# Performance work log

Hardware: AMD Instinct MI355X
Metric: run time of the kernel (lower is better)

The kernel has to match this reference:

```python
import jax, jax.numpy as jnp
import numpy as np

SLOPE = 25.0  # snntorch fast_sigmoid default surrogate slope

@jax.custom_vjp
def spike(u):
    return (u > 0).astype(u.dtype)

def _spike_fwd(u):
    return spike(u), u

def _spike_bwd(u, g):
    return (g / (1.0 + SLOPE * jnp.abs(u)) ** 2,)

spike.defvjp(_spike_fwd, _spike_bwd)

def fake_quant(W):
    # brevitas-style int8 per-tensor symmetric fake-quant with STE
    s = jnp.max(jnp.abs(W)) / 127.0
    q = jnp.clip(jnp.round(W / s), -127.0, 127.0) * s
    return W + jax.lax.stop_gradient(q - W)

def setup_inputs() -> dict:
    key = jax.random.key(0)
    ks = jax.random.split(key, 8)
    B, NIN, T = 256, 512, 256
    H1, H2, OUT = 512, 512, 128
    data = jax.random.normal(ks[0], (B, NIN, T), dtype=jnp.float32)
    W1 = jax.random.normal(ks[1], (H1, NIN), dtype=jnp.float32) / np.sqrt(NIN)
    W2 = jax.random.normal(ks[2], (H2, H1), dtype=jnp.float32) / np.sqrt(H1)
    Wrec = jax.random.normal(ks[3], (H2, H2), dtype=jnp.float32) / np.sqrt(H2)
    W3 = jax.random.normal(ks[4], (OUT, H2), dtype=jnp.float32) / np.sqrt(H2)
    beta = jnp.float32(0.9)
    th = jnp.float32(1.0)
    return {"data": data, "W1": W1, "W2": W2, "Wrec": Wrec, "W3": W3,
            "beta1": beta, "th1": th, "beta_r": beta, "th_r": th,
            "beta2": beta, "th2": th}

def reference(data, W1, W2, Wrec, W3, beta1, th1, beta_r, th_r, beta2, th2):
    B = data.shape[0]
    H1, H2, OUT = W1.shape[0], W2.shape[0], W3.shape[0]
    W1q = fake_quant(W1)
    W2q = fake_quant(W2)
    Wrq = fake_quant(Wrec)
    W3q = fake_quant(W3)
    b1 = jnp.clip(beta1, 0.0, 1.0)
    br = jnp.clip(beta_r, 0.0, 1.0)
    b2 = jnp.clip(beta2, 0.0, 1.0)
    # time-major input: [T, B, NIN]
    xs = jnp.transpose(data, (2, 0, 1))

    def step(carry, x):
        m1, mr, sr, m2 = carry
        # leaky1: reset zero, reset_delay=False
        m1 = b1 * m1 + x @ W1q.T
        s1 = spike(m1 - th1)
        m1 = m1 * (1.0 - s1)
        # recurrent LIF (RLeaky-like), reset zero, reset_delay=True:
        # previous spike resets the membrane at the start of this step
        h = s1 @ W2q.T + sr @ Wrq.T
        mr = (br * mr + h) * (1.0 - sr)
        sr = spike(mr - th_r)
        # leaky2: reset zero, reset_delay=False
        m2 = b2 * m2 + sr @ W3q.T
        s2 = spike(m2 - th2)
        m2 = m2 * (1.0 - s2)
        return (m1, mr, sr, m2), s2

    init = (jnp.zeros((B, H1), jnp.float32),
            jnp.zeros((B, H2), jnp.float32),
            jnp.zeros((B, H2), jnp.float32),
            jnp.zeros((B, OUT), jnp.float32))
    _, spk_rec = jax.lax.scan(step, init, xs)
    return spk_rec  # [T, B, OUT]
```

## Files before the change

kernel.cpp:

```cpp
#include <hip/hip_runtime.h>

#define B_   256
#define NIN_ 512
#define T_   256
#define H1_  512
#define H2_  512
#define OUT_ 128

typedef __attribute__((ext_vector_type(8))) short bf16x8;
typedef __attribute__((ext_vector_type(4))) float f32x4;
typedef __attribute__((address_space(1))) const unsigned int* gl_cu;
typedef __attribute__((address_space(3))) unsigned int* ls_u;

__global__ void absmax_k(const float* __restrict__ W1, const float* __restrict__ W2,
                         const float* __restrict__ Wr, const float* __restrict__ W3,
                         float* __restrict__ scales) {
  const float* W; int n;
  switch (blockIdx.x) {
    case 0:  W = W1; n = H1_ * NIN_; break;
    case 1:  W = W2; n = H2_ * H1_;  break;
    case 2:  W = Wr; n = H2_ * H2_;  break;
    default: W = W3; n = OUT_ * H2_; break;
  }
  int tid = threadIdx.x;
  float m = 0.f;
  const float4* W4 = (const float4*)W;
  int n4 = n >> 2;
  for (int i = tid; i < n4; i += 256) {
    float4 v = W4[i];
    m = fmaxf(m, fmaxf(fmaxf(fabsf(v.x), fabsf(v.y)), fmaxf(fabsf(v.z), fabsf(v.w))));
  }
  __shared__ float red[256];
  red[tid] = m;
  __syncthreads();
  for (int s = 128; s > 0; s >>= 1) {
    if (tid < s) red[tid] = fmaxf(red[tid], red[tid + s]);
    __syncthreads();
  }
  if (tid == 0) scales[blockIdx.x] = red[0] / 127.0f;
}

__global__ void quant_all_k(const float* __restrict__ W1, const float* __restrict__ W2,
                            const float* __restrict__ Wr, const float* __restrict__ W3,
                            const float* __restrict__ scales,
                            float* __restrict__ W1qT, ushort* __restrict__ W2bf,
                            signed char* __restrict__ WrT, ushort* __restrict__ W3bf) {
  const int blk = blockIdx.x;
  if (blk < 1024) {
    int idx = blk * 256 + threadIdx.x;
    int h = idx & (H1_ - 1), i = idx >> 9;
    float s = scales[0];
    float q = rintf(W1[h * NIN_ + i] / s);
    q = fminf(fmaxf(q, -127.f), 127.f);
    W1qT[idx] = q * s;
  } else if (blk < 2048) {
    int idx = (blk - 1024) * 256 + threadIdx.x;
    float s = scales[1];
    float q = rintf(W2[idx] / s);
    q = fminf(fmaxf(q, -127.f), 127.f);
    W2bf[idx] = (ushort)(__float_as_uint(q) >> 16);
  } else if (blk < 3072) {
    int idx = (blk - 2048) * 256 + threadIdx.x;
    int r = idx >> 9, c = idx & (H2_ - 1);
    float s = scales[2];
    float q = rintf(Wr[idx] / s);
    q = fminf(fmaxf(q, -127.f), 127.f);
    WrT[(size_t)c * H2_ + r] = (signed char)q;
  } else {
    int idx = (blk - 3072) * 256 + threadIdx.x;
    float s = scales[3];
    float q = rintf(W3[idx] / s);
    q = fminf(fmaxf(q, -127.f), 127.f);
    W3bf[idx] = (ushort)(__float_as_uint(q) >> 16);
  }
}

__global__ __launch_bounds__(512, 6) void gemm_cur1_k(const float* __restrict__ data,
                                                      const float* __restrict__ W1qT,
                                                      float* __restrict__ cur1) {
  const int b  = blockIdx.y;
  const int t0 = (blockIdx.x >> 2) << 7;
  const int h0 = (blockIdx.x & 3) << 7;
  const int tid = threadIdx.x;

  __shared__ float As[2][16][128];
  __shared__ float Bs[2][16][128];

  const int ty = tid >> 4, tx = tid & 15;
  const int wv = tid >> 6;
  const int ln = tid & 63;

  float acc[4][8];
#pragma unroll
  for (int i = 0; i < 4; i++)
#pragma unroll
    for (int j = 0; j < 8; j++) acc[i][j] = 0.f;

  const float* dbase = data + (size_t)b * NIN_ * T_;

  auto issue = [&](int kb, int buf) {
    const int kr = (wv << 1) + (ln >> 5);
    const float* ga = dbase + (size_t)(kb + kr) * T_ + t0 + ((ln & 31) << 2);
    __builtin_amdgcn_global_load_lds((gl_cu)ga, (ls_u)&As[buf][wv << 1][0], 16, 0, 0);
    const float* gb = W1qT + (size_t)(kb + kr) * H1_ + h0 + ((ln & 31) << 2);
    __builtin_amdgcn_global_load_lds((gl_cu)gb, (ls_u)&Bs[buf][wv << 1][0], 16, 0, 0);
  };

  issue(0, 0);

  for (int p = 0; p < 32; p++) {
    const int cur = p & 1;
    __syncthreads();
    if (p < 31) issue((p + 1) << 4, cur ^ 1);
#pragma unroll
    for (int k = 0; k < 16; k++) {
      float4 A0 = *(const float4*)&As[cur][k][ty * 4];
      float4 B0 = *(const float4*)&Bs[cur][k][tx * 4];
      float4 B1 = *(const float4*)&Bs[cur][k][64 + tx * 4];
      float a[4] = {A0.x, A0.y, A0.z, A0.w};
      float w[8] = {B0.x, B0.y, B0.z, B0.w, B1.x, B1.y, B1.z, B1.w};
#pragma unroll
      for (int i = 0; i < 4; i++)
#pragma unroll
        for (int j = 0; j < 8; j++)
          acc[i][j] = fmaf(a[i], w[j], acc[i][j]);
    }
  }

#pragma unroll
  for (int i = 0; i < 4; i++) {
    int row = ty * 4 + i;
    float* op = cur1 + (size_t)(t0 + row) * (B_ * H1_) + (size_t)b * H1_ + h0;
    float4 cA = {acc[i][0], acc[i][1], acc[i][2], acc[i][3]};
    float4 cB = {acc[i][4], acc[i][5], acc[i][6], acc[i][7]};
    *(float4*)(op + tx * 4)      = cA;
    *(float4*)(op + 64 + tx * 4) = cB;
  }
}

__global__ __launch_bounds__(256) void scan1_k(const float* __restrict__ cur1,
                                               unsigned char* __restrict__ s1u,
                                               const float* __restrict__ beta1p,
                                               const float* __restrict__ th1p) {
  const int n = blockIdx.x * 256 + threadIdx.x;
  const float b1 = fminf(fmaxf(beta1p[0], 0.f), 1.f);
  const float th1 = th1p[0];
  const size_t S = (size_t)B_ * H1_;
  float m1 = 0.f;
  for (int t = 0; t < T_; t += 4) {
    float c0 = cur1[(size_t)t * S + n];
    float c1 = cur1[(size_t)(t + 1) * S + n];
    float c2 = cur1[(size_t)(t + 2) * S + n];
    float c3 = cur1[(size_t)(t + 3) * S + n];
    m1 = b1 * m1 + c0; bool s0 = m1 - th1 > 0.f; if (s0) m1 = 0.f;
    s1u[(size_t)t * S + n] = s0;
    m1 = b1 * m1 + c1; bool s1 = m1 - th1 > 0.f; if (s1) m1 = 0.f;
    s1u[(size_t)(t + 1) * S + n] = s1;
    m1 = b1 * m1 + c2; bool s2 = m1 - th1 > 0.f; if (s2) m1 = 0.f;
    s1u[(size_t)(t + 2) * S + n] = s2;
    m1 = b1 * m1 + c3; bool s3 = m1 - th1 > 0.f; if (s3) m1 = 0.f;
    s1u[(size_t)(t + 3) * S + n] = s3;
  }
}

__global__ __launch_bounds__(256) void gemm_spk_k(const unsigned char* __restrict__ A8,
                                                  const ushort* __restrict__ Bw,
                                                  float* __restrict__ C, int N) {
  __shared__ short As[128 * 72];
  __shared__ short Bs[128 * 72];
  const int tid = threadIdx.x;
  const int m0 = blockIdx.y << 7;
  const int n0 = blockIdx.x << 7;
  const int lane = tid & 63, wave = tid >> 6;
  const int quad = lane >> 4, lm = lane & 15;
  const int wm = wave << 5;

  f32x4 acc[2][8];
#pragma unroll
  for (int s = 0; s < 2; s++)
#pragma unroll
    for (int n = 0; n < 8; n++) acc[s][n] = (f32x4){0.f, 0.f, 0.f, 0.f};

  for (int kb = 0; kb < 512; kb += 64) {
    uint4 av[2], bv[4];
#pragma unroll
    for (int i = 0; i < 2; i++) {
      int ch = tid + (i << 8);
      int row = ch >> 2, offB = (ch & 3) << 4;
      av[i] = *(const uint4*)(A8 + (size_t)(m0 + row) * 512 + kb + offB);
    }
#pragma unroll
    for (int i = 0; i < 4; i++) {
      int ch = tid + (i << 8);
      int row = ch >> 3, off = (ch & 7) << 3;
      bv[i] = *(const uint4*)(Bw + (size_t)(n0 + row) * 512 + kb + off);
    }
    __syncthreads();
#pragma unroll
    for (int i = 0; i < 2; i++) {
      int ch = tid + (i << 8);
      int row = ch >> 2, offB = (ch & 3) << 4;
      unsigned u[4] = {av[i].x, av[i].y, av[i].z, av[i].w};
      unsigned d[8];
#pragma unroll
      for (int w = 0; w < 4; w++) {
        unsigned uu = u[w];
        d[2 * w]     = ((uu & 1u) | ((uu & 0x100u) << 8)) * 0x3F80u;
        d[2 * w + 1] = (((uu >> 16) & 1u) | ((uu & 0x1000000u) >> 8)) * 0x3F80u;
      }
      uint4* dst = (uint4*)&As[row * 72 + offB];
      dst[0] = make_uint4(d[0], d[1], d[2], d[3]);
      dst[1] = make_uint4(d[4], d[5], d[6], d[7]);
    }
#pragma unroll
    for (int i = 0; i < 4; i++) {
      int ch = tid + (i << 8);
      int row = ch >> 3, off = (ch & 7) << 3;
      *(uint4*)&Bs[row * 72 + off] = bv[i];
    }
    __syncthreads();
#pragma unroll
    for (int kc = 0; kc < 64; kc += 32) {
      bf16x8 af0 = *(const bf16x8*)&As[(wm + lm) * 72 + kc + quad * 8];
      bf16x8 af1 = *(const bf16x8*)&As[(wm + 16 + lm) * 72 + kc + quad * 8];
      bf16x8 bfr[8];
#pragma unroll
      for (int n = 0; n < 8; n++)
        bfr[n] = *(const bf16x8*)&Bs[((n << 4) + lm) * 72 + kc + quad * 8];
#pragma unroll
      for (int n = 0; n < 8; n++) {
        acc[0][n] = __builtin_amdgcn_mfma_f32_16x16x32_bf16(af0, bfr[n], acc[0][n], 0, 0, 0);
        acc[1][n] = __builtin_amdgcn_mfma_f32_16x16x32_bf16(af1, bfr[n], acc[1][n], 0, 0, 0);
      }
    }
    __syncthreads();
  }

#pragma unroll
  for (int s = 0; s < 2; s++)
#pragma unroll
    for (int n = 0; n < 8; n++) {
      int row = m0 + wm + (s << 4) + quad * 4;
      int col = n0 + (n << 4) + lm;
#pragma unroll
      for (int r = 0; r < 4; r++)
        C[(size_t)(row + r) * N + col] = acc[s][n][r];
    }
}

__device__ __forceinline__ void unp_add(unsigned w, int* a) {
  int iw = (int)w;
  a[0] += (iw << 24) >> 24;
  a[1] += (iw << 16) >> 24;
  a[2] += (iw << 8) >> 24;
  a[3] += iw >> 24;
}

__global__ __launch_bounds__(1024) void recurrent_k(
    const float* __restrict__ cur2a,
    const signed char* __restrict__ WrT,
    unsigned char* __restrict__ sru,
    const float* __restrict__ scales,
    const float* __restrict__ betarp, const float* __restrict__ thrp) {
  const int b = blockIdx.x;
  const int tid = threadIdx.x;
  const float s2sc = scales[1];
  const float srsc = scales[2];
  const float br = fminf(fmaxf(betarp[0], 0.f), 1.f);
  const float thr = thrp[0];

  const unsigned* WrT4 = (const unsigned*)WrT;

  __shared__ unsigned WrL[256 * 128];
  __shared__ int red[8][H2_];
  __shared__ int lstLo[2][256];
  __shared__ int lstHi[2][256];
  __shared__ int ncLo[2], ncHi[2];

  {
    const uint4* src = (const uint4*)WrT4;
    uint4* dst = (uint4*)WrL;
    for (int i = tid; i < 8192; i += 1024) dst[i] = src[i];
  }
  if (tid < 2) { ncLo[tid] = 0; ncHi[tid] = 0; }
  __syncthreads();

  float mr = 0.f, sr_own = 0.f;
  const int g = tid >> 7;
  const int c = tid & 127;

  for (int t = 0; t < T_; t++) {
    const int old = t & 1, nxt = old ^ 1;
    float c2 = 0.f;
    if (tid < H2_) c2 = cur2a[((size_t)t * B_ + b) * H2_ + tid];
    if (tid == 1022) ncLo[nxt] = 0;
    if (tid == 1023) ncHi[nxt] = 0;
    const int nLo = ncLo[old];
    const int nHi = ncHi[old];
    const int* LLo = lstLo[old];
    const int* LHi = lstHi[old];

    int a4[4] = {0, 0, 0, 0};
    {
      int k = g;
      for (; k + 56 < nLo; k += 64) {
        int i0 = LLo[k],      i1 = LLo[k + 8],  i2 = LLo[k + 16], i3 = LLo[k + 24];
        int i4 = LLo[k + 32], i5 = LLo[k + 40], i6 = LLo[k + 48], i7 = LLo[k + 56];
        unsigned w0 = WrL[(i0 << 7) + c], w1 = WrL[(i1 << 7) + c];
        unsigned w2 = WrL[(i2 << 7) + c], w3 = WrL[(i3 << 7) + c];
        unsigned w4 = WrL[(i4 << 7) + c], w5 = WrL[(i5 << 7) + c];
        unsigned w6 = WrL[(i6 << 7) + c], w7 = WrL[(i7 << 7) + c];
        unp_add(w0, a4); unp_add(w1, a4); unp_add(w2, a4); unp_add(w3, a4);
        unp_add(w4, a4); unp_add(w5, a4); unp_add(w6, a4); unp_add(w7, a4);
      }
      for (; k + 24 < nLo; k += 32) {
        int i0 = LLo[k], i1 = LLo[k + 8], i2 = LLo[k + 16], i3 = LLo[k + 24];
        unsigned w0 = WrL[(i0 << 7) + c], w1 = WrL[(i1 << 7) + c];
        unsigned w2 = WrL[(i2 << 7) + c], w3 = WrL[(i3 << 7) + c];
        unp_add(w0, a4); unp_add(w1, a4); unp_add(w2, a4); unp_add(w3, a4);
      }
      for (; k < nLo; k += 8) unp_add(WrL[(LLo[k] << 7) + c], a4);
    }
    {
      int k = g;
      for (; k + 56 < nHi; k += 64) {
        int i0 = LHi[k],      i1 = LHi[k + 8],  i2 = LHi[k + 16], i3 = LHi[k + 24];
        int i4 = LHi[k + 32], i5 = LHi[k + 40], i6 = LHi[k + 48], i7 = LHi[k + 56];
        unsigned w0 = WrT4[(i0 << 7) + c], w1 = WrT4[(i1 << 7) + c];
        unsigned w2 = WrT4[(i2 << 7) + c], w3 = WrT4[(i3 << 7) + c];
        unsigned w4 = WrT4[(i4 << 7) + c], w5 = WrT4[(i5 << 7) + c];
        unsigned w6 = WrT4[(i6 << 7) + c], w7 = WrT4[(i7 << 7) + c];
        unp_add(w0, a4); unp_add(w1, a4); unp_add(w2, a4); unp_add(w3, a4);
        unp_add(w4, a4); unp_add(w5, a4); unp_add(w6, a4); unp_add(w7, a4);
      }
      for (; k + 24 < nHi; k += 32) {
        int i0 = LHi[k], i1 = LHi[k + 8], i2 = LHi[k + 16], i3 = LHi[k + 24];
        unsigned w0 = WrT4[(i0 << 7) + c], w1 = WrT4[(i1 << 7) + c];
        unsigned w2 = WrT4[(i2 << 7) + c], w3 = WrT4[(i3 << 7) + c];
        unp_add(w0, a4); unp_add(w1, a4); unp_add(w2, a4); unp_add(w3, a4);
      }
      for (; k < nHi; k += 8) unp_add(WrT4[(LHi[k] << 7) + c], a4);
    }
    *(int4*)&red[g][c << 2] = make_int4(a4[0], a4[1], a4[2], a4[3]);
    __syncthreads();

    bool spike = false;
    if (tid < H2_) {
      int acc = red[0][tid] + red[1][tid] + red[2][tid] + red[3][tid]
              + red[4][tid] + red[5][tid] + red[6][tid] + red[7][tid];
      float h = s2sc * c2 + srsc * (float)acc;
      mr = (br * mr + h) * (1.f - sr_own);
      sr_own = (mr - thr > 0.f) ? 1.f : 0.f;
      sru[((size_t)t * B_ + b) * H2_ + tid] = (unsigned char)(sr_own != 0.f);
      spike = (sr_own != 0.f);
    }
    unsigned long long bm = __ballot(spike);
    if (bm != 0ull) {
      const int lane = tid & 63;
      const int ldr = (int)__ffsll((long long)bm) - 1;
      int* cnt = (tid < 256) ? &ncLo[nxt] : &ncHi[nxt];
      int* dst = (tid < 256) ? lstLo[nxt] : lstHi[nxt];
      int base = 0;
      if (lane == ldr) base = atomicAdd(cnt, (int)__popcll(bm));
      base = __shfl(base, ldr);
      if (spike)
        dst[base + (int)__popcll(bm & ((1ull << lane) - 1ull))] = tid;
    }
    __syncthreads();
  }
}

__global__ __launch_bounds__(256) void scan3_k(const float* __restrict__ cur3,
                                               float* __restrict__ out,
                                               const float* __restrict__ scales,
                                               const float* __restrict__ beta2p,
                                               const float* __restrict__ th2p) {
  const int n = blockIdx.x * 256 + threadIdx.x;
  const float s3sc = scales[3];
  const float b2 = fminf(fmaxf(beta2p[0], 0.f), 1.f);
  const float th2 = th2p[0];
  const size_t S = (size_t)B_ * OUT_;
  float m2 = 0.f;
  for (int t = 0; t < T_; t += 4) {
    float v0 = cur3[(size_t)t * S + n];
    float v1 = cur3[(size_t)(t + 1) * S + n];
    float v2 = cur3[(size_t)(t + 2) * S + n];
    float v3 = cur3[(size_t)(t + 3) * S + n];
    m2 = b2 * m2 + s3sc * v0; float p0 = (m2 - th2 > 0.f) ? 1.f : 0.f; m2 *= (1.f - p0);
    out[(size_t)t * S + n] = p0;
    m2 = b2 * m2 + s3sc * v1; float p1 = (m2 - th2 > 0.f) ? 1.f : 0.f; m2 *= (1.f - p1);
    out[(size_t)(t + 1) * S + n] = p1;
    m2 = b2 * m2 + s3sc * v2; float p2 = (m2 - th2 > 0.f) ? 1.f : 0.f; m2 *= (1.f - p2);
    out[(size_t)(t + 2) * S + n] = p2;
    m2 = b2 * m2 + s3sc * v3; float p3 = (m2 - th2 > 0.f) ? 1.f : 0.f; m2 *= (1.f - p3);
    out[(size_t)(t + 3) * S + n] = p3;
  }
}

extern "C" void kernel_launch(void* const* d_in, const int* in_sizes, int n_in,
                              void* d_out, int out_size, void* d_ws, size_t ws_size,
                              hipStream_t stream) {
  const float* data  = (const float*)d_in[0];
  const float* W1    = (const float*)d_in[1];
  const float* W2    = (const float*)d_in[2];
  const float* Wr    = (const float*)d_in[3];
  const float* W3    = (const float*)d_in[4];
  const float* beta1 = (const float*)d_in[5];
  const float* th1   = (const float*)d_in[6];
  const float* betar = (const float*)d_in[7];
  const float* thr   = (const float*)d_in[8];
  const float* beta2 = (const float*)d_in[9];
  const float* th2   = (const float*)d_in[10];

  char* ws = (char*)d_ws;
  float*         scales = (float*)ws;
  float*         W1qT   = (float*)(ws + 4096);
  ushort*        W2bf   = (ushort*)(ws + 4096 + 1048576);
  ushort*        W3bf   = (ushort*)(ws + 4096 + 1048576 + 524288);
  signed char*   WrT    = (signed char*)(ws + 4096 + 1048576 + 524288 + 131072);
  float*         regA   = (float*)(ws + (size_t)4194304);
  unsigned char* regB   = (unsigned char*)(ws + (size_t)4194304 + 134217728);

  float* cur1  = regA;
  float* cur2a = regA;
  float* cur3  = regA;
  unsigned char* s1u = regB;
  unsigned char* sru = regB + (size_t)33554432;

  hipLaunchKernelGGL(absmax_k, dim3(4), dim3(256), 0, stream, W1, W2, Wr, W3, scales);
  hipLaunchKernelGGL(quant_all_k, dim3(3328), dim3(256), 0, stream,
                     W1, W2, Wr, W3, scales, W1qT, W2bf, WrT, W3bf);

  hipLaunchKernelGGL(gemm_cur1_k, dim3(8, 256), dim3(512), 0, stream, data, W1qT, cur1);
  hipLaunchKernelGGL(scan1_k, dim3((B_ * H1_) / 256), dim3(256), 0, stream, cur1, s1u, beta1, th1);
  hipLaunchKernelGGL(gemm_spk_k, dim3(4, 512), dim3(256), 0, stream, s1u, W2bf, cur2a, H2_);
  hipLaunchKernelGGL(recurrent_k, dim3(256), dim3(1024), 0, stream, cur2a, WrT, sru, scales, betar, thr);
  hipLaunchKernelGGL(gemm_spk_k, dim3(1, 512), dim3(256), 0, stream, sru, W3bf, cur3, OUT_);
  hipLaunchKernelGGL(scan3_k, dim3((B_ * OUT_) / 256), dim3(256), 0, stream, cur3, (float*)d_out, scales, beta2, th2);
}
```

Baseline: 1.026 ms.

## Use int8 MFMA for spike GEMMs and vectorize scan1 over four neurons

The spike-times-weight GEMMs now store the quantized W2/W3 as int8 and feed the 0/1 spike bytes straight into the int8 16x16x64 MFMA with int32 accumulation. This removes the per-tile byte-to-bf16 expansion, halves the weight bytes loaded, and halves the MFMA count per K-chunk. Results stay exact because both operands are small integers. Separately, scan1 now has each thread handle four adjacent neurons with float4 loads and uchar4 stores, giving wider memory accesses but a quarter as many threads.

New measurement: 1.083 ms. 1.06x slower.

```diff
diff --git a/kernel.cpp b/kernel.cpp
--- a/kernel.cpp
+++ b/kernel.cpp
@@ -7,8 +7,7 @@
 #define H2_  512
 #define OUT_ 128
 
-typedef __attribute__((ext_vector_type(8))) short bf16x8;
-typedef __attribute__((ext_vector_type(4))) float f32x4;
+typedef __attribute__((ext_vector_type(4))) int i32x4;
 typedef __attribute__((address_space(1))) const unsigned int* gl_cu;
 typedef __attribute__((address_space(3))) unsigned int* ls_u;
 
@@ -43,8 +42,8 @@
 __global__ void quant_all_k(const float* __restrict__ W1, const float* __restrict__ W2,
                             const float* __restrict__ Wr, const float* __restrict__ W3,
                             const float* __restrict__ scales,
-                            float* __restrict__ W1qT, ushort* __restrict__ W2bf,
-                            signed char* __restrict__ WrT, ushort* __restrict__ W3bf) {
+                            float* __restrict__ W1qT, signed char* __restrict__ W2i8,
+                            signed char* __restrict__ WrT, signed char* __restrict__ W3i8) {
   const int blk = blockIdx.x;
   if (blk < 1024) {
     int idx = blk * 256 + threadIdx.x;
@@ -58,7 +57,7 @@
     float s = scales[1];
     float q = rintf(W2[idx] / s);
     q = fminf(fmaxf(q, -127.f), 127.f);
-    W2bf[idx] = (ushort)(__float_as_uint(q) >> 16);
+    W2i8[idx] = (signed char)q;
   } else if (blk < 3072) {
     int idx = (blk - 2048) * 256 + threadIdx.x;
     int r = idx >> 9, c = idx & (H2_ - 1);
@@ -71,7 +70,7 @@
     float s = scales[3];
     float q = rintf(W3[idx] / s);
     q = fminf(fmaxf(q, -127.f), 127.f);
-    W3bf[idx] = (ushort)(__float_as_uint(q) >> 16);
+    W3i8[idx] = (signed char)q;
   }
 }
 
@@ -142,32 +141,28 @@
                                                unsigned char* __restrict__ s1u,
                                                const float* __restrict__ beta1p,
                                                const float* __restrict__ th1p) {
-  const int n = blockIdx.x * 256 + threadIdx.x;
+  const int n0 = (blockIdx.x * 256 + threadIdx.x) << 2;
   const float b1 = fminf(fmaxf(beta1p[0], 0.f), 1.f);
   const float th1 = th1p[0];
   const size_t S = (size_t)B_ * H1_;
-  float m1 = 0.f;
-  for (int t = 0; t < T_; t += 4) {
-    float c0 = cur1[(size_t)t * S + n];
-    float c1 = cur1[(size_t)(t + 1) * S + n];
-    float c2 = cur1[(size_t)(t + 2) * S + n];
-    float c3 = cur1[(size_t)(t + 3) * S + n];
-    m1 = b1 * m1 + c0; bool s0 = m1 - th1 > 0.f; if (s0) m1 = 0.f;
-    s1u[(size_t)t * S + n] = s0;
-    m1 = b1 * m1 + c1; bool s1 = m1 - th1 > 0.f; if (s1) m1 = 0.f;
-    s1u[(size_t)(t + 1) * S + n] = s1;
-    m1 = b1 * m1 + c2; bool s2 = m1 - th1 > 0.f; if (s2) m1 = 0.f;
-    s1u[(size_t)(t + 2) * S + n] = s2;
-    m1 = b1 * m1 + c3; bool s3 = m1 - th1 > 0.f; if (s3) m1 = 0.f;
-    s1u[(size_t)(t + 3) * S + n] = s3;
+  float m0 = 0.f, m1 = 0.f, m2 = 0.f, m3 = 0.f;
+#pragma unroll 2
+  for (int t = 0; t < T_; t++) {
+    float4 c = *(const float4*)(cur1 + (size_t)t * S + n0);
+    uchar4 o;
+    m0 = b1 * m0 + c.x; bool s0 = m0 - th1 > 0.f; if (s0) m0 = 0.f; o.x = s0;
+    m1 = b1 * m1 + c.y; bool s1 = m1 - th1 > 0.f; if (s1) m1 = 0.f; o.y = s1;
+    m2 = b1 * m2 + c.z; bool s2 = m2 - th1 > 0.f; if (s2) m2 = 0.f; o.z = s2;
+    m3 = b1 * m3 + c.w; bool s3 = m3 - th1 > 0.f; if (s3) m3 = 0.f; o.w = s3;
+    *(uchar4*)(s1u + (size_t)t * S + n0) = o;
   }
 }
 
 __global__ __launch_bounds__(256) void gemm_spk_k(const unsigned char* __restrict__ A8,
-                                                  const ushort* __restrict__ Bw,
+                                                  const signed char* __restrict__ Bw,
                                                   float* __restrict__ C, int N) {
-  __shared__ short As[128 * 72];
-  __shared__ short Bs[128 * 72];
+  __shared__ __align__(16) signed char As[128 * 80];
+  __shared__ __align__(16) signed char Bs[128 * 80];
   const int tid = threadIdx.x;
   const int m0 = blockIdx.y << 7;
   const int n0 = blockIdx.x << 7;
@@ -175,63 +170,41 @@
   const int quad = lane >> 4, lm = lane & 15;
   const int wm = wave << 5;
 
-  f32x4 acc[2][8];
+  i32x4 acc[2][8];
 #pragma unroll
   for (int s = 0; s < 2; s++)
 #pragma unroll
-    for (int n = 0; n < 8; n++) acc[s][n] = (f32x4){0.f, 0.f, 0.f, 0.f};
+    for (int n = 0; n < 8; n++) acc[s][n] = (i32x4){0, 0, 0, 0};
+
+  const int row = tid >> 2;
+  const int offB = (tid & 3) << 4;
 
   for (int kb = 0; kb < 512; kb += 64) {
-    uint4 av[2], bv[4];
+    uint4 av[2], bv[2];
 #pragma unroll
     for (int i = 0; i < 2; i++) {
-      int ch = tid + (i << 8);
-      int row = ch >> 2, offB = (ch & 3) << 4;
-      av[i] = *(const uint4*)(A8 + (size_t)(m0 + row) * 512 + kb + offB);
-    }
-#pragma unroll
-    for (int i = 0; i < 4; i++) {
-      int ch = tid + (i << 8);
-      int row = ch >> 3, off = (ch & 7) << 3;
-      bv[i] = *(const uint4*)(Bw + (size_t)(n0 + row) * 512 + kb + off);
+      const int r = row + (i << 6);
+      av[i] = *(const uint4*)(A8 + (size_t)(m0 + r) * 512 + kb + offB);
+      bv[i] = *(const uint4*)(Bw + (size_t)(n0 + r) * 512 + kb + offB);
     }
     __syncthreads();
 #pragma unroll
     for (int i = 0; i < 2; i++) {
-      int ch = tid + (i << 8);
-      int row = ch >> 2, offB = (ch & 3) << 4;
-      unsigned u[4] = {av[i].x, av[i].y, av[i].z, av[i].w};
-      unsigned d[8];
-#pragma unroll
-      for (int w = 0; w < 4; w++) {
-        unsigned uu = u[w];
-        d[2 * w]     = ((uu & 1u) | ((uu & 0x100u) << 8)) * 0x3F80u;
-        d[2 * w + 1] = (((uu >> 16) & 1u) | ((uu & 0x1000000u) >> 8)) * 0x3F80u;
-      }
-      uint4* dst = (uint4*)&As[row * 72 + offB];
-      dst[0] = make_uint4(d[0], d[1], d[2], d[3]);
-      dst[1] = make_uint4(d[4], d[5], d[6], d[7]);
-    }
-#pragma unroll
-    for (int i = 0; i < 4; i++) {
-      int ch = tid + (i << 8);
-      int row = ch >> 3, off = (ch & 7) << 3;
-      *(uint4*)&Bs[row * 72 + off] = bv[i];
-    }
-    __syncthreads();
-#pragma unroll
-    for (int kc = 0; kc < 64; kc += 32) {
-      bf16x8 af0 = *(const bf16x8*)&As[(wm + lm) * 72 + kc + quad * 8];
-      bf16x8 af1 = *(const bf16x8*)&As[(wm + 16 + lm) * 72 + kc + quad * 8];
-      bf16x8 bfr[8];
-#pragma unroll
-      for (int n = 0; n < 8; n++)
-        bfr[n] = *(const bf16x8*)&Bs[((n << 4) + lm) * 72 + kc + quad * 8];
-#pragma unroll
-      for (int n = 0; n < 8; n++) {
-        acc[0][n] = __builtin_amdgcn_mfma_f32_16x16x32_bf16(af0, bfr[n], acc[0][n], 0, 0, 0);
-        acc[1][n] = __builtin_amdgcn_mfma_f32_16x16x32_bf16(af1, bfr[n], acc[1][n], 0, 0, 0);
-      }
+      const int r = row + (i << 6);
+      *(uint4*)&As[r * 80 + offB] = av[i];
+      *(uint4*)&Bs[r * 80 + offB] = bv[i];
+    }
+    __syncthreads();
+    i32x4 a0 = *(const i32x4*)&As[(wm + lm) * 80 + (quad << 4)];
+    i32x4 a1 = *(const i32x4*)&As[(wm + 16 + lm) * 80 + (quad << 4)];
+    i32x4 bq[8];
+#pragma unroll
+    for (int n = 0; n < 8; n++)
+      bq[n] = *(const i32x4*)&Bs[((n << 4) + lm) * 80 + (quad << 4)];
+#pragma unroll
+    for (int n = 0; n < 8; n++) {
+      acc[0][n] = __builtin_amdgcn_mfma_i32_16x16x64_i8(a0, bq[n], acc[0][n], 0, 0, 0);
+      acc[1][n] = __builtin_amdgcn_mfma_i32_16x16x64_i8(a1, bq[n], acc[1][n], 0, 0, 0);
     }
     __syncthreads();
   }
@@ -240,11 +213,11 @@
   for (int s = 0; s < 2; s++)
 #pragma unroll
     for (int n = 0; n < 8; n++) {
-      int row = m0 + wm + (s << 4) + quad * 4;
+      int orow = m0 + wm + (s << 4) + quad * 4;
       int col = n0 + (n << 4) + lm;
 #pragma unroll
       for (int r = 0; r < 4; r++)
-        C[(size_t)(row + r) * N + col] = acc[s][n][r];
+        C[(size_t)(orow + r) * N + col] = (float)acc[s][n][r];
     }
 }
 
@@ -415,8 +388,8 @@
   char* ws = (char*)d_ws;
   float*         scales = (float*)ws;
   float*         W1qT   = (float*)(ws + 4096);
-  ushort*        W2bf   = (ushort*)(ws + 4096 + 1048576);
-  ushort*        W3bf   = (ushort*)(ws + 4096 + 1048576 + 524288);
+  signed char*   W2i8   = (signed char*)(ws + 4096 + 1048576);
+  signed char*   W3i8   = (signed char*)(ws + 4096 + 1048576 + 524288);
   signed char*   WrT    = (signed char*)(ws + 4096 + 1048576 + 524288 + 131072);
   float*         regA   = (float*)(ws + (size_t)4194304);
   unsigned char* regB   = (unsigned char*)(ws + (size_t)4194304 + 134217728);
@@ -429,12 +402,12 @@
 
   hipLaunchKernelGGL(absmax_k, dim3(4), dim3(256), 0, stream, W1, W2, Wr, W3, scales);
   hipLaunchKernelGGL(quant_all_k, dim3(3328), dim3(256), 0, stream,
-                     W1, W2, Wr, W3, scales, W1qT, W2bf, WrT, W3bf);
+                     W1, W2, Wr, W3, scales, W1qT, W2i8, WrT, W3i8);
 
   hipLaunchKernelGGL(gemm_cur1_k, dim3(8, 256), dim3(512), 0, stream, data, W1qT, cur1);
-  hipLaunchKernelGGL(scan1_k, dim3((B_ * H1_) / 256), dim3(256), 0, stream, cur1, s1u, beta1, th1);
-  hipLaunchKernelGGL(gemm_spk_k, dim3(4, 512), dim3(256), 0, stream, s1u, W2bf, cur2a, H2_);
+  hipLaunchKernelGGL(scan1_k, dim3((B_ * H1_) / 1024), dim3(256), 0, stream, cur1, s1u, beta1, th1);
+  hipLaunchKernelGGL(gemm_spk_k, dim3(4, 512), dim3(256), 0, stream, s1u, W2i8, cur2a, H2_);
   hipLaunchKernelGGL(recurrent_k, dim3(256), dim3(1024), 0, stream, cur2a, WrT, sru, scales, betar, thr);
-  hipLaunchKernelGGL(gemm_spk_k, dim3(1, 512), dim3(256), 0, stream, sru, W3bf, cur3, OUT_);
+  hipLaunchKernelGGL(gemm_spk_k, dim3(1, 512), dim3(256), 0, stream, sru, W3i8, cur3, OUT_);
   hipLaunchKernelGGL(scan3_k, dim3((B_ * OUT_) / 256), dim3(256), 0, stream, cur3, (float*)d_out, scales, beta2, th2);
 }
```
